# Kernel tuning notes

Measured on AMD Instinct MI355X. Metric: run time of the kernel, lower is better.

Reference implementation:

```python
import jax, jax.numpy as jnp
import numpy as np

EPS = 1e-5

def _layernorm(h):
    # parameter-free LayerNorm over last dim (elementwise_affine=False)
    mu = jnp.mean(h, axis=-1, keepdims=True)
    var = jnp.mean(jnp.square(h - mu), axis=-1, keepdims=True)
    return (h - mu) / jnp.sqrt(var + EPS)

def setup_inputs() -> dict:
    key = jax.random.key(0)
    k1, k2, k3, k4 = jax.random.split(key, 4)
    B, D, F_, I = 16, 37, 4096, 64
    x = jax.random.normal(k1, (B, D, F_), dtype=jnp.float32)
    s = 1.0 / np.sqrt(D)  # ~ torch Linear default init scale
    Wq = jax.random.normal(k2, (D, I), dtype=jnp.float32) * s
    Wk = jax.random.normal(k3, (D, I), dtype=jnp.float32) * s
    Wv = jax.random.normal(k4, (D, I), dtype=jnp.float32) * s
    return {"x": x, "Wq": Wq, "Wk": Wk, "Wv": Wv}

def reference(x, Wq, Wk, Wv):
    # x: [B, depth, featuresize] -> entities [B, F, depth]
    xb = jnp.transpose(x, (0, 2, 1))
    q = _layernorm(jnp.einsum('bfd,di->bfi', xb, Wq))
    k = _layernorm(jnp.einsum('bfd,di->bfi', xb, Wk))
    v = _layernorm(jnp.einsum('bfd,di->bfi', xb, Wv))
    d = q.shape[-1]
    att = jnp.einsum('bqi,bki->bqk', q, k) / jnp.sqrt(jnp.float32(d))
    # faithful to torch: softmax over dim=1 (the query axis), not the key axis
    weights = jax.nn.softmax(att, axis=-2)
    return jnp.einsum('bqk,bki->bqi', weights, v)
```

## Files before the change

### kernel.cpp

```cpp
#include <hip/hip_runtime.h>
#include <math.h>

#define B_  16
#define D_  37
#define F_  4096
#define I_  64
#define EPS 1e-5f
#define QSCALE 0.18033688011112042f
#define NQS 2

typedef unsigned short u16;
typedef __bf16 bf16x8 __attribute__((ext_vector_type(8)));
typedef __bf16 bf16x2v __attribute__((ext_vector_type(2)));
typedef float  f32x16 __attribute__((ext_vector_type(16)));
typedef float  f32x2v __attribute__((ext_vector_type(2)));
typedef unsigned int u32x4 __attribute__((ext_vector_type(4)));
typedef int i32x2 __attribute__((ext_vector_type(2)));

#define ZERO16 {0,0,0,0, 0,0,0,0, 0,0,0,0, 0,0,0,0}
#define MFMA32(a, b, c) __builtin_amdgcn_mfma_f32_32x32x16_bf16((a), (b), (c), 0, 0, 0)

#if __has_builtin(__builtin_amdgcn_exp2f)
#define EX2(x) __builtin_amdgcn_exp2f(x)
#else
#define EX2(x) exp2f(x)
#endif
#if __has_builtin(__builtin_amdgcn_rcpf)
#define RCP(x) __builtin_amdgcn_rcpf(x)
#else
#define RCP(x) (1.f / (x))
#endif

__device__ __forceinline__ u16 f2b(float f) {
  unsigned u = __builtin_bit_cast(unsigned, f);
  return (u16)((u + 0x7fffu + ((u >> 16) & 1u)) >> 16);
}
__device__ __forceinline__ unsigned pk2(float lo, float hi) {
  f32x2v f = {lo, hi};
  bf16x2v h = __builtin_convertvector(f, bf16x2v);
  return __builtin_bit_cast(unsigned, h);
}

__device__ __forceinline__ void plswap(unsigned& a, unsigned& b) {
#if __has_builtin(__builtin_amdgcn_permlane32_swap)
  i32x2 r = __builtin_amdgcn_permlane32_swap((int)a, (int)b, false, false);
  a = (unsigned)r[0];
  b = (unsigned)r[1];
#else
  const int lh = (int)((threadIdx.x & 63) >> 5);
  unsigned pa = (unsigned)__shfl_xor((int)a, 32, 64);
  unsigned pb = (unsigned)__shfl_xor((int)b, 32, 64);
  unsigned na = lh ? pb : a;
  unsigned nb = lh ? b : pa;
  a = na;
  b = nb;
#endif
}

__device__ __forceinline__ void build_af(const f32x16& s, bf16x8& f0, bf16x8& f1) {
  float e[16];
#pragma unroll
  for (int r = 0; r < 16; ++r) e[r] = EX2(s[r]);
  unsigned a = pk2(e[0], e[1]),   bq = pk2(e[2], e[3]);
  unsigned c = pk2(e[4], e[5]),   d  = pk2(e[6], e[7]);
  plswap(a, c);
  plswap(bq, d);
  u32x4 v0 = {a, bq, c, d};
  f0 = __builtin_bit_cast(bf16x8, v0);
  unsigned ee = pk2(e[8], e[9]),  ff = pk2(e[10], e[11]);
  unsigned g  = pk2(e[12], e[13]), h = pk2(e[14], e[15]);
  plswap(ee, g);
  plswap(ff, h);
  u32x4 v1 = {ee, ff, g, h};
  f1 = __builtin_bit_cast(bf16x8, v1);
}

__device__ __forceinline__ bf16x8 ldfrag(const u16* base, int row, int kb) {
  return *(const bf16x8*)(base + (row << 6) + ((kb ^ (row & 7)) << 3));
}
__device__ __forceinline__ void stage16(u16* dst, const u16* src, int c, int spitch) {
  const int r = c >> 3, cb = c & 7;
  const int4 v = *(const int4*)(src + (size_t)r * spitch + (cb << 3));
  *(int4*)(dst + (r << 6) + ((cb ^ (r & 7)) << 3)) = v;
}
__device__ __forceinline__ int soff_l(int c) {
  const int r = c >> 3, cb = c & 7;
  return (r << 6) + ((cb ^ (r & 7)) << 3);
}
__device__ __forceinline__ int soff_g(int c, int spitch) {
  return (c >> 3) * spitch + ((c & 7) << 3);
}

__global__ __launch_bounds__(256) void qkv_ln_k(
    const float* __restrict__ x,
    const float* __restrict__ Wq, const float* __restrict__ Wk,
    const float* __restrict__ Wv,
    u16* __restrict__ qn, u16* __restrict__ kn, u16* __restrict__ vt) {
  __shared__ float sW[3 * D_ * I_];
  __shared__ float xs[D_ * 64];
  __shared__ __align__(16) u16 vtile[64 * 72];

  const int t = threadIdx.x;
  const int b = blockIdx.y;
  const int f0 = blockIdx.x * 64;

  for (int i = t; i < D_ * I_; i += 256) {
    sW[i]               = Wq[i];
    sW[D_ * I_ + i]     = Wk[i];
    sW[2 * D_ * I_ + i] = Wv[i];
  }
  const float* xb = x + (size_t)b * D_ * F_ + f0;
  for (int i = t; i < D_ * 64; i += 256)
    xs[i] = xb[(size_t)(i >> 6) * F_ + (i & 63)];
  __syncthreads();

  const int lane = t & 63, w = t >> 6;

  for (int it = 0; it < 16; ++it) {
    const int fl = w * 16 + it;
    float hq = 0.f, hk = 0.f, hv = 0.f;
#pragma unroll
    for (int d = 0; d < D_; ++d) {
      const float xv = xs[d * 64 + fl];
      hq = fmaf(xv, sW[d * 64 + lane], hq);
      hk = fmaf(xv, sW[D_ * I_ + d * 64 + lane], hk);
      hv = fmaf(xv, sW[2 * D_ * I_ + d * 64 + lane], hv);
    }
    auto lnorm = [&](float a) -> float {
      float s = a;
#pragma unroll
      for (int o = 32; o > 0; o >>= 1) s += __shfl_xor(s, o, 64);
      const float mu = s * (1.f / 64.f);
      const float d0 = a - mu;
      float v = d0 * d0;
#pragma unroll
      for (int o = 32; o > 0; o >>= 1) v += __shfl_xor(v, o, 64);
      return d0 * rsqrtf(v * (1.f / 64.f) + EPS);
    };
    const size_t fo = ((size_t)b * F_ + f0 + fl) * I_ + lane;
    qn[fo] = f2b(lnorm(hq) * QSCALE);
    kn[fo] = f2b(lnorm(hk));
    vtile[lane * 72 + fl] = f2b(lnorm(hv));
  }
  __syncthreads();
  for (int p = 0; p < 2; ++p) {
    const int c = p * 256 + t;
    const int r = c >> 3, off = (c & 7) * 8;
    const int4 v = *(const int4*)&vtile[r * 72 + off];
    *(int4*)(vt + ((size_t)b * I_ + r) * F_ + f0 + off) = v;
  }
}

__global__ __launch_bounds__(256, 2) void attn_stats_k(
    const u16* __restrict__ qn, const u16* __restrict__ kn,
    float* __restrict__ zp) {
  __shared__ __align__(16) u16 sm[16384];

  const int t = threadIdx.x, lane = t & 63, w = t >> 6;
  const int l31 = lane & 31, lh = lane >> 5;
  const int b = blockIdx.y, k0 = blockIdx.x * 256, qh = blockIdx.z;

  const u16* kb = kn + ((size_t)b * F_ + k0) * I_;
#pragma unroll
  for (int p = 0; p < 8; ++p) stage16(sm, kb, p * 256 + t, 64);
  __syncthreads();
  bf16x8 kf[2][4];
#pragma unroll
  for (int kb2 = 0; kb2 < 2; ++kb2)
#pragma unroll
    for (int ic = 0; ic < 4; ++ic)
      kf[kb2][ic] = ldfrag(sm + (w * 64 + kb2 * 32) * 64, l31, ic * 2 + lh);
  __syncthreads();

  int qoff_l[2], qoff_g[2];
#pragma unroll
  for (int p = 0; p < 2; ++p) {
    const int c = p * 256 + t;
    qoff_l[p] = soff_l(c);
    qoff_g[p] = soff_g(c, 64);
  }

  const u16* qsrc = qn + ((size_t)b * F_ + qh * (F_ / NQS)) * I_;
#pragma unroll
  for (int p = 0; p < 2; ++p)
    *(int4*)(sm + qoff_l[p]) = *(const int4*)(qsrc + qoff_g[p]);
  qsrc += 64 * I_;

  float Zc[2][2] = {{0.f, 0.f}, {0.f, 0.f}};
  const int NC = F_ / NQS / 64;

  for (int c = 0; c < NC; ++c) {
    const int cur = (c & 1) * 4096;
    __syncthreads();
    if (c + 1 < NC) {
      const int nxt = cur ^ 4096;
#pragma unroll
      for (int p = 0; p < 2; ++p)
        *(int4*)(sm + nxt + qoff_l[p]) = *(const int4*)(qsrc + qoff_g[p]);
      qsrc += 64 * I_;
    }

    f32x16 a00 = ZERO16, a01 = ZERO16, a10 = ZERO16, a11 = ZERO16;
#pragma unroll
    for (int ic = 0; ic < 4; ++ic) {
      const bf16x8 q0f = ldfrag(sm + cur, l31, ic * 2 + lh);
      const bf16x8 q1f = ldfrag(sm + cur + 32 * 64, l31, ic * 2 + lh);
      a00 = MFMA32(q0f, kf[0][ic], a00);
      a01 = MFMA32(q0f, kf[1][ic], a01);
      a10 = MFMA32(q1f, kf[0][ic], a10);
      a11 = MFMA32(q1f, kf[1][ic], a11);
    }
#pragma unroll
    for (int r = 0; r < 16; ++r) {
      Zc[0][0] += EX2(a00[r]);
      Zc[0][1] += EX2(a01[r]);
      Zc[1][0] += EX2(a10[r]);
      Zc[1][1] += EX2(a11[r]);
    }
  }

#pragma unroll
  for (int kb2 = 0; kb2 < 2; ++kb2) {
    float Zt = Zc[0][kb2] + Zc[1][kb2];
    Zt += __shfl_xor(Zt, 32, 64);
    if (lane < 32)
      zp[((size_t)qh * B_ + b) * F_ + k0 + w * 64 + kb2 * 32 + lane] = Zt;
  }
}

__global__ __launch_bounds__(256) void vscale_k(u16* __restrict__ vt,
                                                const float* __restrict__ zp) {
  const int b = blockIdx.y;
  const int off = (blockIdx.x * 256 + (int)threadIdx.x) * 8;
  const int k = off & (F_ - 1);
  u16* p = vt + (size_t)b * I_ * F_ + off;
  const float* z0 = zp + (size_t)b * F_ + k;
  const float* z1 = zp + (size_t)B_ * F_ + (size_t)b * F_ + k;
  int4 raw = *(const int4*)p;
  u16 es[8], os[8];
  *(int4*)es = raw;
#pragma unroll
  for (int j = 0; j < 8; ++j) {
    const float v = __builtin_bit_cast(float, (unsigned)es[j] << 16);
    const float rz = RCP(z0[j] + z1[j]);
    os[j] = f2b(v * rz);
  }
  *(int4*)p = *(int4*)os;
}

__global__ __launch_bounds__(128, 2) void attn_out_k(
    const u16* __restrict__ qn, const u16* __restrict__ kn,
    const u16* __restrict__ vt, float* __restrict__ out) {
  __shared__ __align__(16) u16 sm[16384];

  const int t = threadIdx.x, lane = t & 63, w = t >> 6;
  const int l31 = lane & 31, lh = lane >> 5;
  const int b = blockIdx.y, q0 = blockIdx.x * 128;

  const u16* qb = qn + ((size_t)b * F_ + q0) * I_;
#pragma unroll
  for (int p = 0; p < 8; ++p) stage16(sm, qb, p * 128 + t, 64);
  __syncthreads();
  bf16x8 qf[2][4];
#pragma unroll
  for (int qb2 = 0; qb2 < 2; ++qb2)
#pragma unroll
    for (int ic = 0; ic < 4; ++ic)
      qf[qb2][ic] = ldfrag(sm + (w * 64 + qb2 * 32) * 64, l31, ic * 2 + lh);
  __syncthreads();

  int off_l[4], kg[4], vg[4];
#pragma unroll
  for (int p = 0; p < 4; ++p) {
    const int c = p * 128 + t;
    off_l[p] = soff_l(c);
    kg[p] = soff_g(c, 64);
    vg[p] = soff_g(c, F_);
  }

  const u16* ksrc = kn + (size_t)b * F_ * I_;
  const u16* vsrc = vt + (size_t)b * I_ * F_;
#pragma unroll
  for (int p = 0; p < 4; ++p) {
    *(int4*)(sm + off_l[p])        = *(const int4*)(ksrc + kg[p]);
    *(int4*)(sm + 8192 + off_l[p]) = *(const int4*)(vsrc + vg[p]);
  }
  ksrc += 64 * I_;
  vsrc += 64;

  f32x16 o00 = ZERO16, o01 = ZERO16, o10 = ZERO16, o11 = ZERO16;
  const int NC = F_ / 64;

  for (int c = 0; c < NC; ++c) {
    const int cur = (c & 1) * 4096;
    __syncthreads();
    if (c + 1 < NC) {
      const int nxt = cur ^ 4096;
#pragma unroll
      for (int p = 0; p < 4; ++p) {
        *(int4*)(sm + nxt + off_l[p])        = *(const int4*)(ksrc + kg[p]);
        *(int4*)(sm + 8192 + nxt + off_l[p]) = *(const int4*)(vsrc + vg[p]);
      }
      ksrc += 64 * I_;
      vsrc += 64;
    }

    const u16* Kc = sm + cur;
    f32x16 s00 = ZERO16, s01 = ZERO16, s10 = ZERO16, s11 = ZERO16;
#pragma unroll
    for (int ic = 0; ic < 4; ++ic) {
      const bf16x8 ak0 = ldfrag(Kc, l31, ic * 2 + lh);
      const bf16x8 ak1 = ldfrag(Kc + 32 * 64, l31, ic * 2 + lh);
      s00 = MFMA32(ak0, qf[0][ic], s00);
      s01 = MFMA32(ak0, qf[1][ic], s01);
      s10 = MFMA32(ak1, qf[0][ic], s10);
      s11 = MFMA32(ak1, qf[1][ic], s11);
    }

    bf16x8 af[2][4];
    build_af(s00, af[0][0], af[0][1]);
    build_af(s10, af[0][2], af[0][3]);
    build_af(s01, af[1][0], af[1][1]);
    build_af(s11, af[1][2], af[1][3]);

    const u16* Vc = sm + 8192 + cur;
#pragma unroll
    for (int kb4 = 0; kb4 < 4; ++kb4) {
      const bf16x8 bv0 = ldfrag(Vc, l31, kb4 * 2 + lh);
      const bf16x8 bv1 = ldfrag(Vc + 32 * 64, l31, kb4 * 2 + lh);
      o00 = MFMA32(af[0][kb4], bv0, o00);
      o01 = MFMA32(af[0][kb4], bv1, o01);
      o10 = MFMA32(af[1][kb4], bv0, o10);
      o11 = MFMA32(af[1][kb4], bv1, o11);
    }
  }

  float* ob = out + ((size_t)b * F_ + q0 + w * 64) * I_;
#pragma unroll
  for (int r = 0; r < 16; ++r) {
    const int qr = (r & 3) + 8 * (r >> 2) + 4 * lh;
    ob[(size_t)qr * I_ + l31]              = o00[r];
    ob[(size_t)qr * I_ + 32 + l31]         = o01[r];
    ob[(size_t)(32 + qr) * I_ + l31]       = o10[r];
    ob[(size_t)(32 + qr) * I_ + 32 + l31]  = o11[r];
  }
}

extern "C" void kernel_launch(void* const* d_in, const int* in_sizes, int n_in,
                              void* d_out, int out_size, void* d_ws,
                              size_t ws_size, hipStream_t stream) {
  const float* x  = (const float*)d_in[0];
  const float* Wq = (const float*)d_in[1];
  const float* Wk = (const float*)d_in[2];
  const float* Wv = (const float*)d_in[3];
  float* out = (float*)d_out;

  const size_t NBF = (size_t)B_ * F_ * I_;
  u16* qn   = (u16*)d_ws;
  u16* kn   = qn + NBF;
  u16* vt   = kn + NBF;
  float* zp = (float*)(vt + NBF);

  qkv_ln_k<<<dim3(F_ / 64, B_), 256, 0, stream>>>(x, Wq, Wk, Wv, qn, kn, vt);
  attn_stats_k<<<dim3(F_ / 256, B_, NQS), 256, 0, stream>>>(qn, kn, zp);
  vscale_k<<<dim3(I_ * F_ / 2048, B_), 256, 0, stream>>>(vt, zp);
  attn_out_k<<<dim3(F_ / 128, B_), 128, 0, stream>>>(qn, kn, vt, out);
}
```

Baseline: 273.5 us.

## Split attention output over key halves with bf16 partials and reduction kernel

Splits the key/value loop of the attention output kernel across two blocks along a new grid dimension, doubling the block count. One half writes fp32 output directly and the other writes a bf16 partial, which a new elementwise kernel adds into the output. This aims to raise parallelism and improve CU load balance, at the cost of extra global traffic, an extra launch, and bf16 rounding of half the accumulation.

```diff
diff --git a/kernel.cpp b/kernel.cpp
--- a/kernel.cpp
+++ b/kernel.cpp
@@ -34,6 +34,9 @@
 __device__ __forceinline__ u16 f2b(float f) {
   unsigned u = __builtin_bit_cast(unsigned, f);
   return (u16)((u + 0x7fffu + ((u >> 16) & 1u)) >> 16);
+}
+__device__ __forceinline__ float b2f(u16 h) {
+  return __builtin_bit_cast(float, (unsigned)h << 16);
 }
 __device__ __forceinline__ unsigned pk2(float lo, float hi) {
   f32x2v f = {lo, hi};
@@ -241,7 +244,7 @@
   *(int4*)es = raw;
 #pragma unroll
   for (int j = 0; j < 8; ++j) {
-    const float v = __builtin_bit_cast(float, (unsigned)es[j] << 16);
+    const float v = b2f(es[j]);
     const float rz = RCP(z0[j] + z1[j]);
     os[j] = f2b(v * rz);
   }
@@ -250,12 +253,13 @@
 
 __global__ __launch_bounds__(128, 2) void attn_out_k(
     const u16* __restrict__ qn, const u16* __restrict__ kn,
-    const u16* __restrict__ vt, float* __restrict__ out) {
+    const u16* __restrict__ vt, float* __restrict__ out,
+    u16* __restrict__ pout) {
   __shared__ __align__(16) u16 sm[16384];
 
   const int t = threadIdx.x, lane = t & 63, w = t >> 6;
   const int l31 = lane & 31, lh = lane >> 5;
-  const int b = blockIdx.y, q0 = blockIdx.x * 128;
+  const int b = blockIdx.y, q0 = blockIdx.x * 128, ks = blockIdx.z;
 
   const u16* qb = qn + ((size_t)b * F_ + q0) * I_;
 #pragma unroll
@@ -278,8 +282,8 @@
     vg[p] = soff_g(c, F_);
   }
 
-  const u16* ksrc = kn + (size_t)b * F_ * I_;
-  const u16* vsrc = vt + (size_t)b * I_ * F_;
+  const u16* ksrc = kn + ((size_t)b * F_ + ks * (F_ / 2)) * I_;
+  const u16* vsrc = vt + (size_t)b * I_ * F_ + ks * (F_ / 2);
 #pragma unroll
   for (int p = 0; p < 4; ++p) {
     *(int4*)(sm + off_l[p])        = *(const int4*)(ksrc + kg[p]);
@@ -289,7 +293,7 @@
   vsrc += 64;
 
   f32x16 o00 = ZERO16, o01 = ZERO16, o10 = ZERO16, o11 = ZERO16;
-  const int NC = F_ / 64;
+  const int NC = F_ / 2 / 64;
 
   for (int c = 0; c < NC; ++c) {
     const int cur = (c & 1) * 4096;
@@ -335,15 +339,41 @@
     }
   }
 
-  float* ob = out + ((size_t)b * F_ + q0 + w * 64) * I_;
-#pragma unroll
-  for (int r = 0; r < 16; ++r) {
-    const int qr = (r & 3) + 8 * (r >> 2) + 4 * lh;
-    ob[(size_t)qr * I_ + l31]              = o00[r];
-    ob[(size_t)qr * I_ + 32 + l31]         = o01[r];
-    ob[(size_t)(32 + qr) * I_ + l31]       = o10[r];
-    ob[(size_t)(32 + qr) * I_ + 32 + l31]  = o11[r];
-  }
+  if (ks == 0) {
+    float* ob = out + ((size_t)b * F_ + q0 + w * 64) * I_;
+#pragma unroll
+    for (int r = 0; r < 16; ++r) {
+      const int qr = (r & 3) + 8 * (r >> 2) + 4 * lh;
+      ob[(size_t)qr * I_ + l31]              = o00[r];
+      ob[(size_t)qr * I_ + 32 + l31]         = o01[r];
+      ob[(size_t)(32 + qr) * I_ + l31]       = o10[r];
+      ob[(size_t)(32 + qr) * I_ + 32 + l31]  = o11[r];
+    }
+  } else {
+    u16* pb = pout + ((size_t)b * F_ + q0 + w * 64) * I_;
+#pragma unroll
+    for (int r = 0; r < 16; ++r) {
+      const int qr = (r & 3) + 8 * (r >> 2) + 4 * lh;
+      pb[(size_t)qr * I_ + l31]              = f2b(o00[r]);
+      pb[(size_t)qr * I_ + 32 + l31]         = f2b(o01[r]);
+      pb[(size_t)(32 + qr) * I_ + l31]       = f2b(o10[r]);
+      pb[(size_t)(32 + qr) * I_ + 32 + l31]  = f2b(o11[r]);
+    }
+  }
+}
+
+__global__ __launch_bounds__(256) void reduce_k(float* __restrict__ out,
+                                                const u16* __restrict__ pout) {
+  const size_t i = ((size_t)blockIdx.x * 256 + threadIdx.x) * 8;
+  float4 a0 = *(const float4*)(out + i);
+  float4 a1 = *(const float4*)(out + i + 4);
+  int4 praw = *(const int4*)(pout + i);
+  u16 es[8];
+  *(int4*)es = praw;
+  a0.x += b2f(es[0]); a0.y += b2f(es[1]); a0.z += b2f(es[2]); a0.w += b2f(es[3]);
+  a1.x += b2f(es[4]); a1.y += b2f(es[5]); a1.z += b2f(es[6]); a1.w += b2f(es[7]);
+  *(float4*)(out + i)     = a0;
+  *(float4*)(out + i + 4) = a1;
 }
 
 extern "C" void kernel_launch(void* const* d_in, const int* in_sizes, int n_in,
@@ -360,9 +390,11 @@
   u16* kn   = qn + NBF;
   u16* vt   = kn + NBF;
   float* zp = (float*)(vt + NBF);
+  u16* pout = (u16*)(zp + (size_t)NQS * B_ * F_);
 
   qkv_ln_k<<<dim3(F_ / 64, B_), 256, 0, stream>>>(x, Wq, Wk, Wv, qn, kn, vt);
   attn_stats_k<<<dim3(F_ / 256, B_, NQS), 256, 0, stream>>>(qn, kn, zp);
   vscale_k<<<dim3(I_ * F_ / 2048, B_), 256, 0, stream>>>(vt, zp);
-  attn_out_k<<<dim3(F_ / 128, B_), 128, 0, stream>>>(qn, kn, vt, out);
-}
+  attn_out_k<<<dim3(F_ / 128, B_, 2), 128, 0, stream>>>(qn, kn, vt, out, pout);
+  reduce_k<<<dim3((int)(NBF / 2048)), 256, 0, stream>>>(out, pout);
+}
```

Measured after the change: 241.8 us. 1.13x faster.
